# Kernel optimization log

Measured on AMD Instinct MI355X. Metric: run time of the kernel, lower is better.

Reference implementation:

```python
import jax, jax.numpy as jnp
import numpy as np

N, E, IN, HID, OUT = 100000, 1600000, 128, 128, 64


def _gcn(x, w, b, src, dst, norm, n):
    # PyG GCNConv: linear transform, then normalized scatter-add aggregation
    h = x @ w                                  # [N, F_out]
    msg = h[src] * norm[:, None]               # gather + scale, [E', F_out]
    agg = jax.ops.segment_sum(msg, dst, num_segments=n)
    return agg + b


def setup_inputs() -> dict:
    key = jax.random.key(0)
    ks = jax.random.split(key, 10)
    s = 0.05
    return {
        "X": jax.random.normal(ks[0], (N, IN), jnp.float32),
        "edge_index": jax.random.randint(ks[1], (2, E), 0, N, jnp.int64),
        "unused": 0,
        "gw1": jax.random.normal(ks[2], (IN, HID), jnp.float32) * s,
        "gb1": jnp.zeros((HID,), jnp.float32),
        "lw1": jax.random.normal(ks[3], (IN, HID), jnp.float32) * s,
        "lb1": jnp.zeros((HID,), jnp.float32),
        "gw2": jax.random.normal(ks[4], (HID, HID), jnp.float32) * s,
        "gb2": jnp.zeros((HID,), jnp.float32),
        "lw2": jax.random.normal(ks[5], (HID, HID), jnp.float32) * s,
        "lb2": jnp.zeros((HID,), jnp.float32),
        "gw3": jax.random.normal(ks[6], (HID, HID), jnp.float32) * s,
        "gb3": jnp.zeros((HID,), jnp.float32),
        "lw3": jax.random.normal(ks[7], (HID, HID), jnp.float32) * s,
        "lb3": jnp.zeros((HID,), jnp.float32),
        "fcw": jax.random.normal(ks[8], (HID, OUT), jnp.float32) * s,
        "fcb": jnp.zeros((OUT,), jnp.float32),
    }


def reference(X, edge_index, unused, gw1, gb1, lw1, lb1, gw2, gb2, lw2, lb2,
              gw3, gb3, lw3, lb3, fcw, fcb):
    n = X.shape[0]
    loop = jnp.arange(n)
    src = jnp.concatenate([edge_index[0], loop])   # self-loops appended
    dst = jnp.concatenate([edge_index[1], loop])
    deg = jax.ops.segment_sum(jnp.ones_like(dst, dtype=X.dtype), dst, num_segments=n)
    dis = jnp.where(deg > 0, jax.lax.rsqrt(jnp.maximum(deg, 1e-12)), 0.0)
    norm = dis[src] * dis[dst]                     # D^-1/2 (A+I) D^-1/2 weights

    lrelu = lambda v: jax.nn.leaky_relu(v, negative_slope=0.01)
    h = lrelu(_gcn(X, gw1, gb1, src, dst, norm, n) + X @ lw1 + lb1)
    h = lrelu(_gcn(h, gw2, gb2, src, dst, norm, n) + h @ lw2 + lb2)
    h = lrelu(_gcn(h, gw3, gb3, src, dst, norm, n) + h @ lw3 + lb3)
    y = h @ fcw + fcb
    return (h, y)
```

## Files before the change

### kernel.cpp

```cpp
#include <hip/hip_runtime.h>
#include <cstdint>
#include <cstddef>


typedef __attribute__((ext_vector_type(4))) float f32x4;
typedef __attribute__((ext_vector_type(8))) short bf16x8;
typedef unsigned short u16;

#define G_CHUNKS 256

__device__ __forceinline__ float bf2f(unsigned int u) {
  union { unsigned int i; float f; } v;
  v.i = u << 16;
  return v.f;
}
__device__ __forceinline__ u16 f2bf(float f) {
  union { float f; unsigned int i; } v;
  v.f = f;
  unsigned int i = v.i;
  return (u16)((i + 0x7FFFu + ((i >> 16) & 1u)) >> 16);
}


__global__ __launch_bounds__(256) void k_hist(const int* __restrict__ ei,
                                              int* __restrict__ ghist,
                                              int E, int B, int chunk) {
  __shared__ int h[512];
  for (int t = threadIdx.x; t < B; t += 256) h[t] = 0;
  __syncthreads();
  const int g = blockIdx.x;
  const int beg = g * chunk;
  const int end = min(beg + chunk, E);
  for (int e = beg + threadIdx.x; e < end; e += 256)
    atomicAdd(&h[ei[E + e] >> 8], 1);
  __syncthreads();
  for (int t = threadIdx.x; t < B; t += 256) ghist[(size_t)t * G_CHUNKS + g] = h[t];
}

__global__ __launch_bounds__(256) void k_hscan(int* __restrict__ ghist,
                                               int* __restrict__ btot) {
  __shared__ int sm[256];
  int* p = ghist + (size_t)blockIdx.x * G_CHUNKS;
  const int t = threadIdx.x;
  int v = p[t];
  sm[t] = v;
  __syncthreads();
  for (int off = 1; off < 256; off <<= 1) {
    int u = (t >= off) ? sm[t - off] : 0;
    __syncthreads();
    sm[t] += u;
    __syncthreads();
  }
  p[t] = sm[t] - v;
  if (t == 255) btot[blockIdx.x] = sm[255];
}

__global__ __launch_bounds__(512) void k_bscan(const int* __restrict__ btot,
                                               int* __restrict__ boff, int B,
                                               int* __restrict__ rowptr, int n,
                                               int E, int tot) {
  __shared__ int sm[512];
  const int t = threadIdx.x;
  int v = (t < B) ? btot[t] : 0;
  sm[t] = v;
  __syncthreads();
  for (int off = 1; off < 512; off <<= 1) {
    int u = (t >= off) ? sm[t - off] : 0;
    __syncthreads();
    sm[t] += u;
    __syncthreads();
  }
  if (t < B) boff[t] = sm[t] - v;
  if (t == 0) {
    boff[B] = E;
    rowptr[n] = tot;
  }
}

__global__ __launch_bounds__(256) void k_scatter(const int* __restrict__ ei,
                                                 const int* __restrict__ ghist,
                                                 const int* __restrict__ boff,
                                                 unsigned int* __restrict__ ebuf,
                                                 int E, int B, int chunk) {
  __shared__ int off[512];
  const int g = blockIdx.x;
  for (int t = threadIdx.x; t < B; t += 256)
    off[t] = boff[t] + ghist[(size_t)t * G_CHUNKS + g];
  __syncthreads();
  const int beg = g * chunk;
  const int end = min(beg + chunk, E);
  for (int e = beg + threadIdx.x; e < end; e += 256) {
    int s = ei[e];
    int d = ei[E + e];
    int pos = atomicAdd(&off[d >> 8], 1);
    ebuf[pos] = ((unsigned int)s << 8) | (unsigned int)(d & 255);
  }
}

__global__ __launch_bounds__(256) void k_cfill(const unsigned int* __restrict__ ebuf,
                                               const int* __restrict__ boff,
                                               int* __restrict__ rowptr,
                                               int* __restrict__ col,
                                               float* __restrict__ dis, int n) {
  __shared__ int cnt[256];
  __shared__ int fl[256];
  const int b = blockIdx.x;
  const int t = threadIdx.x;
  const int beg = boff[b];
  const int end = boff[b + 1];
  const int node0 = b << 8;
  const int nn = min(256, n - node0);
  cnt[t] = 0;
  __syncthreads();
  for (int e = beg + t; e < end; e += 256)
    atomicAdd(&cnt[ebuf[e] & 255u], 1);
  __syncthreads();
  int v = cnt[t];
  __shared__ int sm[256];
  sm[t] = v;
  __syncthreads();
  for (int off = 1; off < 256; off <<= 1) {
    int u = (t >= off) ? sm[t - off] : 0;
    __syncthreads();
    sm[t] += u;
    __syncthreads();
  }
  if (t < nn) {
    int excl = sm[t] - v;
    int rbase = beg + node0 + t + excl;
    int i = node0 + t;
    rowptr[i] = rbase;
    col[rbase] = i;
    fl[t] = rbase + 1;
    dis[i] = rsqrtf((float)(v + 1));
  }
  __syncthreads();
  for (int e = beg + t; e < end; e += 256) {
    unsigned int pk = ebuf[e];
    int pos = atomicAdd(&fl[pk & 255u], 1);
    col[pos] = (int)(pk >> 8);
  }
}


__global__ __launch_bounds__(256) void k_cvt(const float* __restrict__ src,
                                             u16* __restrict__ dst, int total8) {
  int i = blockIdx.x * 256 + threadIdx.x;
  if (i >= total8) return;
  size_t b = (size_t)i * 8;
  float4 a0 = *(const float4*)(src + b);
  float4 a1 = *(const float4*)(src + b + 4);
  u16 o[8] = {f2bf(a0.x), f2bf(a0.y), f2bf(a0.z), f2bf(a0.w),
              f2bf(a1.x), f2bf(a1.y), f2bf(a1.z), f2bf(a1.w)};
  *(ulonglong2*)(dst + b) = *(ulonglong2*)o;
}

__global__ __launch_bounds__(128) void k_prep(const float* __restrict__ w0,
                                              const float* __restrict__ w1,
                                              const float* __restrict__ w2,
                                              const float* __restrict__ w3,
                                              const float* __restrict__ w4,
                                              const float* __restrict__ w5,
                                              const float* __restrict__ g1,
                                              const float* __restrict__ l1,
                                              const float* __restrict__ g2,
                                              const float* __restrict__ l2,
                                              const float* __restrict__ g3,
                                              const float* __restrict__ l3,
                                              const float* __restrict__ fcw,
                                              u16* __restrict__ wt,
                                              float* __restrict__ bias,
                                              u16* __restrict__ fcT) {
  int bx = blockIdx.x;
  if (bx < 768) {
    int z = bx >> 7, nr = bx & 127, k = threadIdx.x;
    const float* Ws[6] = {w0, w1, w2, w3, w4, w5};
    wt[(size_t)z * 16384 + nr * 128 + k] = f2bf(Ws[z][k * 128 + nr]);
  } else if (bx < 771) {
    int t = (bx - 768) * 128 + threadIdx.x;
    if (t < 384) {
      const float* gs[3] = {g1, g2, g3};
      const float* ls[3] = {l1, l2, l3};
      bias[t] = gs[t >> 7][t & 127] + ls[t >> 7][t & 127];
    }
  } else {
    int nr = bx - 771;
    int k = threadIdx.x;
    fcT[nr * 128 + k] = f2bf(fcw[k * 64 + nr]);
  }
}

__global__ __launch_bounds__(256) void k_spmv_bf(const int* __restrict__ rowptr,
                                                 const int* __restrict__ col,
                                                 const float* __restrict__ dis,
                                                 const u16* __restrict__ Xb,
                                                 u16* __restrict__ SXb, int n) {
  const int wave = threadIdx.x >> 6;
  const int lane = threadIdx.x & 63;
  const int i = blockIdx.x * 4 + wave;
  if (i >= n) return;
  int j = rowptr[i];
  const int end = rowptr[i + 1];
  float ax = 0.f, ay = 0.f;

  for (; (j & 3) && j < end; ++j) {
    int c0 = col[j];
    float w0 = dis[c0];
    unsigned int q0 = *(const unsigned int*)(Xb + (size_t)c0 * 128 + lane * 2);
    ax = fmaf(bf2f(q0 & 0xffffu), w0, ax);
    ay = fmaf(bf2f(q0 >> 16), w0, ay);
  }
  for (; j + 3 < end; j += 4) {
    int4 c4 = *(const int4*)(col + j);
    float w0 = dis[c4.x], w1 = dis[c4.y], w2 = dis[c4.z], w3 = dis[c4.w];
    unsigned int q0 = *(const unsigned int*)(Xb + (size_t)c4.x * 128 + lane * 2);
    unsigned int q1 = *(const unsigned int*)(Xb + (size_t)c4.y * 128 + lane * 2);
    unsigned int q2 = *(const unsigned int*)(Xb + (size_t)c4.z * 128 + lane * 2);
    unsigned int q3 = *(const unsigned int*)(Xb + (size_t)c4.w * 128 + lane * 2);
    ax = fmaf(bf2f(q0 & 0xffffu), w0, ax);
    ay = fmaf(bf2f(q0 >> 16), w0, ay);
    ax = fmaf(bf2f(q1 & 0xffffu), w1, ax);
    ay = fmaf(bf2f(q1 >> 16), w1, ay);
    ax = fmaf(bf2f(q2 & 0xffffu), w2, ax);
    ay = fmaf(bf2f(q2 >> 16), w2, ay);
    ax = fmaf(bf2f(q3 & 0xffffu), w3, ax);
    ay = fmaf(bf2f(q3 >> 16), w3, ay);
  }
  for (; j < end; ++j) {
    int c0 = col[j];
    float w0 = dis[c0];
    unsigned int q0 = *(const unsigned int*)(Xb + (size_t)c0 * 128 + lane * 2);
    ax = fmaf(bf2f(q0 & 0xffffu), w0, ax);
    ay = fmaf(bf2f(q0 >> 16), w0, ay);
  }
  float di = dis[i];
  ax *= di;
  ay *= di;
  unsigned int o = (unsigned int)f2bf(ax) | ((unsigned int)f2bf(ay) << 16);
  *(unsigned int*)(SXb + (size_t)i * 128 + lane * 2) = o;
}

__global__ __launch_bounds__(256) void k_mfma(const u16* __restrict__ A0,
                                              const u16* __restrict__ A1,
                                              const u16* __restrict__ W0T,
                                              const u16* __restrict__ W1T,
                                              const float* __restrict__ bias,
                                              u16* __restrict__ outb,
                                              float* __restrict__ outf, int M) {
  const int lane = threadIdx.x & 63;
  const int wv = threadIdx.x >> 6;
  const int row0 = blockIdx.x * 128 + wv * 32;
  const int r = lane & 15;
  const int kg = lane >> 4;

  f32x4 acc[2][8];
#pragma unroll
  for (int a = 0; a < 2; ++a)
#pragma unroll
    for (int j = 0; j < 8; ++j) acc[a][j] = (f32x4){0.f, 0.f, 0.f, 0.f};

  const int ra0 = min(row0 + r, M - 1);
  const int ra1 = min(row0 + 16 + r, M - 1);

#pragma unroll
  for (int p = 0; p < 2; ++p) {
    const u16* A = p ? A1 : A0;
    const u16* WT = p ? W1T : W0T;
#pragma unroll
    for (int kk = 0; kk < 4; ++kk) {
      const int k0 = kk * 32 + kg * 8;
      bf16x8 a0 = *(const bf16x8*)(A + (size_t)ra0 * 128 + k0);
      bf16x8 a1 = *(const bf16x8*)(A + (size_t)ra1 * 128 + k0);
#pragma unroll
      for (int j = 0; j < 8; ++j) {
        bf16x8 b = *(const bf16x8*)(WT + (size_t)(j * 16 + r) * 128 + k0);
        acc[0][j] = __builtin_amdgcn_mfma_f32_16x16x32_bf16(a0, b, acc[0][j], 0, 0, 0);
        acc[1][j] = __builtin_amdgcn_mfma_f32_16x16x32_bf16(a1, b, acc[1][j], 0, 0, 0);
      }
    }
  }

#pragma unroll
  for (int rf = 0; rf < 2; ++rf)
#pragma unroll
    for (int e = 0; e < 4; ++e) {
      const int row = row0 + rf * 16 + kg * 4 + e;
      if (row >= M) continue;
#pragma unroll
      for (int j = 0; j < 8; ++j) {
        const int c = j * 16 + r;
        float v = acc[rf][j][e] + bias[c];
        v = (v > 0.f) ? v : 0.01f * v;
        if (outf) outf[(size_t)row * 128 + c] = v;
        if (outb) outb[(size_t)row * 128 + c] = f2bf(v);
      }
    }
}

__global__ __launch_bounds__(256) void k_fc_mfma(const u16* __restrict__ hb3,
                                                 const u16* __restrict__ fcT,
                                                 const float* __restrict__ fcb,
                                                 float* __restrict__ y, int M) {
  const int lane = threadIdx.x & 63;
  const int wv = threadIdx.x >> 6;
  const int row0 = blockIdx.x * 128 + wv * 32;
  const int r = lane & 15;
  const int kg = lane >> 4;

  f32x4 acc[2][4];
#pragma unroll
  for (int a = 0; a < 2; ++a)
#pragma unroll
    for (int j = 0; j < 4; ++j) acc[a][j] = (f32x4){0.f, 0.f, 0.f, 0.f};

  const int ra0 = min(row0 + r, M - 1);
  const int ra1 = min(row0 + 16 + r, M - 1);

#pragma unroll
  for (int kk = 0; kk < 4; ++kk) {
    const int k0 = kk * 32 + kg * 8;
    bf16x8 a0 = *(const bf16x8*)(hb3 + (size_t)ra0 * 128 + k0);
    bf16x8 a1 = *(const bf16x8*)(hb3 + (size_t)ra1 * 128 + k0);
#pragma unroll
    for (int j = 0; j < 4; ++j) {
      bf16x8 b = *(const bf16x8*)(fcT + (size_t)(j * 16 + r) * 128 + k0);
      acc[0][j] = __builtin_amdgcn_mfma_f32_16x16x32_bf16(a0, b, acc[0][j], 0, 0, 0);
      acc[1][j] = __builtin_amdgcn_mfma_f32_16x16x32_bf16(a1, b, acc[1][j], 0, 0, 0);
    }
  }

#pragma unroll
  for (int rf = 0; rf < 2; ++rf)
#pragma unroll
    for (int e = 0; e < 4; ++e) {
      const int row = row0 + rf * 16 + kg * 4 + e;
      if (row >= M) continue;
#pragma unroll
      for (int j = 0; j < 4; ++j) {
        const int c = j * 16 + r;
        y[(size_t)row * 64 + c] = acc[rf][j][e] + fcb[c];
      }
    }
}


extern "C" void kernel_launch(void* const* d_in, const int* in_sizes, int n_in,
                              void* d_out, int out_size, void* d_ws, size_t ws_size,
                              hipStream_t stream) {
  const float* X  = (const float*)d_in[0];
  const int* ei   = (const int*)d_in[1];
  const float* gw1 = (const float*)d_in[3];
  const float* gb1 = (const float*)d_in[4];
  const float* lw1 = (const float*)d_in[5];
  const float* lb1 = (const float*)d_in[6];
  const float* gw2 = (const float*)d_in[7];
  const float* gb2 = (const float*)d_in[8];
  const float* lw2 = (const float*)d_in[9];
  const float* lb2 = (const float*)d_in[10];
  const float* gw3 = (const float*)d_in[11];
  const float* gb3 = (const float*)d_in[12];
  const float* lw3 = (const float*)d_in[13];
  const float* lb3 = (const float*)d_in[14];
  const float* fcw = (const float*)d_in[15];
  const float* fcb = (const float*)d_in[16];

  const int n = in_sizes[0] / 128;
  const int E = in_sizes[1] / 2;
  const int tot = E + n;
  const int B = (n + 255) >> 8;
  const int chunk = (E + G_CHUNKS - 1) / G_CHUNKS;

  char* ws = (char*)d_ws;
  size_t off = 0;
  auto alloc = [&](size_t bytes) -> void* {
    void* p = ws + off;
    off = (off + bytes + 255) & ~(size_t)255;
    return p;
  };
  int* ghist   = (int*)alloc((size_t)B * G_CHUNKS * 4);
  int* btot    = (int*)alloc(512 * 4);
  int* boff    = (int*)alloc((size_t)(B + 1) * 4);
  int* rowptr  = (int*)alloc((size_t)(n + 1) * 4);
  float* dis   = (float*)alloc((size_t)n * 4);
  int* col     = (int*)alloc((size_t)tot * 4);
  unsigned int* ebuf = (unsigned int*)alloc((size_t)E * 4);
  u16* Xb      = (u16*)alloc((size_t)n * 128 * 2);
  u16* SXb     = (u16*)alloc((size_t)n * 128 * 2);
  u16* WT      = (u16*)alloc((size_t)6 * 16384 * 2);
  u16* fcT     = (u16*)alloc((size_t)64 * 128 * 2);
  float* bias  = (float*)alloc(384 * 4);

  float* outh = (float*)d_out;
  float* outy = outh + (size_t)n * 128;
  u16* hb = (u16*)outy;

  const int gM = (n + 127) / 128;
  const int gW = (n + 3) / 4;
  const int g8 = (n * 128 / 8 + 255) / 256;

  k_hist<<<G_CHUNKS, 256, 0, stream>>>(ei, ghist, E, B, chunk);
  k_hscan<<<B, 256, 0, stream>>>(ghist, btot);
  k_bscan<<<1, 512, 0, stream>>>(btot, boff, B, rowptr, n, E, tot);
  k_scatter<<<G_CHUNKS, 256, 0, stream>>>(ei, ghist, boff, ebuf, E, B, chunk);
  k_cfill<<<B, 256, 0, stream>>>(ebuf, boff, rowptr, col, dis, n);

  k_cvt<<<g8, 256, 0, stream>>>(X, Xb, n * 128 / 8);
  k_prep<<<835, 128, 0, stream>>>(gw1, lw1, gw2, lw2, gw3, lw3,
                                  gb1, lb1, gb2, lb2, gb3, lb3, fcw,
                                  WT, bias, fcT);

  k_spmv_bf<<<gW, 256, 0, stream>>>(rowptr, col, dis, Xb, SXb, n);
  k_mfma<<<gM, 256, 0, stream>>>(SXb, Xb, WT, WT + 16384, bias, hb, nullptr, n);
  k_spmv_bf<<<gW, 256, 0, stream>>>(rowptr, col, dis, hb, SXb, n);
  k_mfma<<<gM, 256, 0, stream>>>(SXb, hb, WT + 2 * 16384, WT + 3 * 16384,
                                 bias + 128, hb, nullptr, n);
  k_spmv_bf<<<gW, 256, 0, stream>>>(rowptr, col, dis, hb, SXb, n);
  k_mfma<<<gM, 256, 0, stream>>>(SXb, hb, WT + 4 * 16384, WT + 5 * 16384,
                                 bias + 256, Xb, outh, n);
  k_fc_mfma<<<gM, 256, 0, stream>>>(Xb, fcT, fcb, outy, n);
}
```

Baseline: 522.5 us.

## Fuse SpMV aggregation into MFMA layer kernel via swizzled LDS tile

Merges the per-layer SpMV gather kernel and the dense MFMA kernel into one k_layer kernel. Each block aggregates its 128 rows into a swizzled 32KB shared-memory tile, then feeds that tile straight into the MFMA stage. This removes the global write and re-read of the intermediate SX buffer and one launch per layer. The cost is that only 782 blocks of 256 threads do the irregular gather, down from 25k small blocks, so latency hiding for the gather may suffer. A separate h2b buffer is added so a layer never reads and writes the same array.

```diff
diff --git a/kernel.cpp b/kernel.cpp
--- a/kernel.cpp
+++ b/kernel.cpp
@@ -190,66 +190,68 @@
   }
 }
 
-__global__ __launch_bounds__(256) void k_spmv_bf(const int* __restrict__ rowptr,
-                                                 const int* __restrict__ col,
-                                                 const float* __restrict__ dis,
-                                                 const u16* __restrict__ Xb,
-                                                 u16* __restrict__ SXb, int n) {
-  const int wave = threadIdx.x >> 6;
-  const int lane = threadIdx.x & 63;
-  const int i = blockIdx.x * 4 + wave;
-  if (i >= n) return;
-  int j = rowptr[i];
-  const int end = rowptr[i + 1];
-  float ax = 0.f, ay = 0.f;
-
-  for (; (j & 3) && j < end; ++j) {
-    int c0 = col[j];
-    float w0 = dis[c0];
-    unsigned int q0 = *(const unsigned int*)(Xb + (size_t)c0 * 128 + lane * 2);
-    ax = fmaf(bf2f(q0 & 0xffffu), w0, ax);
-    ay = fmaf(bf2f(q0 >> 16), w0, ay);
-  }
-  for (; j + 3 < end; j += 4) {
-    int4 c4 = *(const int4*)(col + j);
-    float w0 = dis[c4.x], w1 = dis[c4.y], w2 = dis[c4.z], w3 = dis[c4.w];
-    unsigned int q0 = *(const unsigned int*)(Xb + (size_t)c4.x * 128 + lane * 2);
-    unsigned int q1 = *(const unsigned int*)(Xb + (size_t)c4.y * 128 + lane * 2);
-    unsigned int q2 = *(const unsigned int*)(Xb + (size_t)c4.z * 128 + lane * 2);
-    unsigned int q3 = *(const unsigned int*)(Xb + (size_t)c4.w * 128 + lane * 2);
-    ax = fmaf(bf2f(q0 & 0xffffu), w0, ax);
-    ay = fmaf(bf2f(q0 >> 16), w0, ay);
-    ax = fmaf(bf2f(q1 & 0xffffu), w1, ax);
-    ay = fmaf(bf2f(q1 >> 16), w1, ay);
-    ax = fmaf(bf2f(q2 & 0xffffu), w2, ax);
-    ay = fmaf(bf2f(q2 >> 16), w2, ay);
-    ax = fmaf(bf2f(q3 & 0xffffu), w3, ax);
-    ay = fmaf(bf2f(q3 >> 16), w3, ay);
-  }
-  for (; j < end; ++j) {
-    int c0 = col[j];
-    float w0 = dis[c0];
-    unsigned int q0 = *(const unsigned int*)(Xb + (size_t)c0 * 128 + lane * 2);
-    ax = fmaf(bf2f(q0 & 0xffffu), w0, ax);
-    ay = fmaf(bf2f(q0 >> 16), w0, ay);
-  }
-  float di = dis[i];
-  ax *= di;
-  ay *= di;
-  unsigned int o = (unsigned int)f2bf(ax) | ((unsigned int)f2bf(ay) << 16);
-  *(unsigned int*)(SXb + (size_t)i * 128 + lane * 2) = o;
-}
-
-__global__ __launch_bounds__(256) void k_mfma(const u16* __restrict__ A0,
-                                              const u16* __restrict__ A1,
-                                              const u16* __restrict__ W0T,
-                                              const u16* __restrict__ W1T,
-                                              const float* __restrict__ bias,
-                                              u16* __restrict__ outb,
-                                              float* __restrict__ outf, int M) {
+__global__ __launch_bounds__(256, 4) void k_layer(const int* __restrict__ rowptr,
+                                                  const int* __restrict__ col,
+                                                  const float* __restrict__ dis,
+                                                  const u16* __restrict__ Ab,
+                                                  const u16* __restrict__ W0T,
+                                                  const u16* __restrict__ W1T,
+                                                  const float* __restrict__ bias,
+                                                  u16* __restrict__ outb,
+                                                  float* __restrict__ outf,
+                                                  int n) {
+  __shared__ char ldsb[128 * 256];
   const int lane = threadIdx.x & 63;
   const int wv = threadIdx.x >> 6;
-  const int row0 = blockIdx.x * 128 + wv * 32;
+  const int row0 = blockIdx.x * 128;
+
+  for (int t = 0; t < 32; ++t) {
+    const int li = wv * 32 + t;
+    const int i = row0 + li;
+    float ax = 0.f, ay = 0.f;
+    if (i < n) {
+      int j = rowptr[i];
+      const int end = rowptr[i + 1];
+      for (; (j & 3) && j < end; ++j) {
+        int c0 = col[j];
+        float w0 = dis[c0];
+        unsigned int q0 = *(const unsigned int*)(Ab + (size_t)c0 * 128 + lane * 2);
+        ax = fmaf(bf2f(q0 & 0xffffu), w0, ax);
+        ay = fmaf(bf2f(q0 >> 16), w0, ay);
+      }
+      for (; j + 3 < end; j += 4) {
+        int4 c4 = *(const int4*)(col + j);
+        float w0 = dis[c4.x], w1 = dis[c4.y], w2 = dis[c4.z], w3 = dis[c4.w];
+        unsigned int q0 = *(const unsigned int*)(Ab + (size_t)c4.x * 128 + lane * 2);
+        unsigned int q1 = *(const unsigned int*)(Ab + (size_t)c4.y * 128 + lane * 2);
+        unsigned int q2 = *(const unsigned int*)(Ab + (size_t)c4.z * 128 + lane * 2);
+        unsigned int q3 = *(const unsigned int*)(Ab + (size_t)c4.w * 128 + lane * 2);
+        ax = fmaf(bf2f(q0 & 0xffffu), w0, ax);
+        ay = fmaf(bf2f(q0 >> 16), w0, ay);
+        ax = fmaf(bf2f(q1 & 0xffffu), w1, ax);
+        ay = fmaf(bf2f(q1 >> 16), w1, ay);
+        ax = fmaf(bf2f(q2 & 0xffffu), w2, ax);
+        ay = fmaf(bf2f(q2 >> 16), w2, ay);
+        ax = fmaf(bf2f(q3 & 0xffffu), w3, ax);
+        ay = fmaf(bf2f(q3 >> 16), w3, ay);
+      }
+      for (; j < end; ++j) {
+        int c0 = col[j];
+        float w0 = dis[c0];
+        unsigned int q0 = *(const unsigned int*)(Ab + (size_t)c0 * 128 + lane * 2);
+        ax = fmaf(bf2f(q0 & 0xffffu), w0, ax);
+        ay = fmaf(bf2f(q0 >> 16), w0, ay);
+      }
+      float di = dis[i];
+      ax *= di;
+      ay *= di;
+    }
+    unsigned int o = (unsigned int)f2bf(ax) | ((unsigned int)f2bf(ay) << 16);
+    const int kbyte = lane * 4;
+    *(unsigned int*)(ldsb + li * 256 + (kbyte ^ ((li & 7) << 4))) = o;
+  }
+  __syncthreads();
+
   const int r = lane & 15;
   const int kg = lane >> 4;
 
@@ -259,24 +261,35 @@
 #pragma unroll
     for (int j = 0; j < 8; ++j) acc[a][j] = (f32x4){0.f, 0.f, 0.f, 0.f};
 
-  const int ra0 = min(row0 + r, M - 1);
-  const int ra1 = min(row0 + 16 + r, M - 1);
-
-#pragma unroll
-  for (int p = 0; p < 2; ++p) {
-    const u16* A = p ? A1 : A0;
-    const u16* WT = p ? W1T : W0T;
-#pragma unroll
-    for (int kk = 0; kk < 4; ++kk) {
-      const int k0 = kk * 32 + kg * 8;
-      bf16x8 a0 = *(const bf16x8*)(A + (size_t)ra0 * 128 + k0);
-      bf16x8 a1 = *(const bf16x8*)(A + (size_t)ra1 * 128 + k0);
-#pragma unroll
-      for (int j = 0; j < 8; ++j) {
-        bf16x8 b = *(const bf16x8*)(WT + (size_t)(j * 16 + r) * 128 + k0);
-        acc[0][j] = __builtin_amdgcn_mfma_f32_16x16x32_bf16(a0, b, acc[0][j], 0, 0, 0);
-        acc[1][j] = __builtin_amdgcn_mfma_f32_16x16x32_bf16(a1, b, acc[1][j], 0, 0, 0);
-      }
+  const int lr0 = wv * 32 + r;
+  const int lr1 = wv * 32 + 16 + r;
+  const int ra0 = min(row0 + lr0, n - 1);
+  const int ra1 = min(row0 + lr1, n - 1);
+  const int sw = (r & 7) << 4;
+
+#pragma unroll
+  for (int kk = 0; kk < 4; ++kk) {
+    const int kb = kk * 64 + kg * 16;
+    bf16x8 a0 = *(const bf16x8*)(ldsb + lr0 * 256 + (kb ^ sw));
+    bf16x8 a1 = *(const bf16x8*)(ldsb + lr1 * 256 + (kb ^ sw));
+    const int k0 = kk * 32 + kg * 8;
+#pragma unroll
+    for (int j = 0; j < 8; ++j) {
+      bf16x8 b = *(const bf16x8*)(W0T + (size_t)(j * 16 + r) * 128 + k0);
+      acc[0][j] = __builtin_amdgcn_mfma_f32_16x16x32_bf16(a0, b, acc[0][j], 0, 0, 0);
+      acc[1][j] = __builtin_amdgcn_mfma_f32_16x16x32_bf16(a1, b, acc[1][j], 0, 0, 0);
+    }
+  }
+#pragma unroll
+  for (int kk = 0; kk < 4; ++kk) {
+    const int k0 = kk * 32 + kg * 8;
+    bf16x8 a0 = *(const bf16x8*)(Ab + (size_t)ra0 * 128 + k0);
+    bf16x8 a1 = *(const bf16x8*)(Ab + (size_t)ra1 * 128 + k0);
+#pragma unroll
+    for (int j = 0; j < 8; ++j) {
+      bf16x8 b = *(const bf16x8*)(W1T + (size_t)(j * 16 + r) * 128 + k0);
+      acc[0][j] = __builtin_amdgcn_mfma_f32_16x16x32_bf16(a0, b, acc[0][j], 0, 0, 0);
+      acc[1][j] = __builtin_amdgcn_mfma_f32_16x16x32_bf16(a1, b, acc[1][j], 0, 0, 0);
     }
   }
 
@@ -284,8 +297,8 @@
   for (int rf = 0; rf < 2; ++rf)
 #pragma unroll
     for (int e = 0; e < 4; ++e) {
-      const int row = row0 + rf * 16 + kg * 4 + e;
-      if (row >= M) continue;
+      const int row = row0 + wv * 32 + rf * 16 + kg * 4 + e;
+      if (row >= n) continue;
 #pragma unroll
       for (int j = 0; j < 8; ++j) {
         const int c = j * 16 + r;
@@ -385,7 +398,7 @@
   int* col     = (int*)alloc((size_t)tot * 4);
   unsigned int* ebuf = (unsigned int*)alloc((size_t)E * 4);
   u16* Xb      = (u16*)alloc((size_t)n * 128 * 2);
-  u16* SXb     = (u16*)alloc((size_t)n * 128 * 2);
+  u16* h2b     = (u16*)alloc((size_t)n * 128 * 2);
   u16* WT      = (u16*)alloc((size_t)6 * 16384 * 2);
   u16* fcT     = (u16*)alloc((size_t)64 * 128 * 2);
   float* bias  = (float*)alloc(384 * 4);
@@ -395,7 +408,6 @@
   u16* hb = (u16*)outy;
 
   const int gM = (n + 127) / 128;
-  const int gW = (n + 3) / 4;
   const int g8 = (n * 128 / 8 + 255) / 256;
 
   k_hist<<<G_CHUNKS, 256, 0, stream>>>(ei, ghist, E, B, chunk);
@@ -409,13 +421,13 @@
                                   gb1, lb1, gb2, lb2, gb3, lb3, fcw,
                                   WT, bias, fcT);
 
-  k_spmv_bf<<<gW, 256, 0, stream>>>(rowptr, col, dis, Xb, SXb, n);
-  k_mfma<<<gM, 256, 0, stream>>>(SXb, Xb, WT, WT + 16384, bias, hb, nullptr, n);
-  k_spmv_bf<<<gW, 256, 0, stream>>>(rowptr, col, dis, hb, SXb, n);
-  k_mfma<<<gM, 256, 0, stream>>>(SXb, hb, WT + 2 * 16384, WT + 3 * 16384,
-                                 bias + 128, hb, nullptr, n);
-  k_spmv_bf<<<gW, 256, 0, stream>>>(rowptr, col, dis, hb, SXb, n);
-  k_mfma<<<gM, 256, 0, stream>>>(SXb, hb, WT + 4 * 16384, WT + 5 * 16384,
-                                 bias + 256, Xb, outh, n);
+  k_layer<<<gM, 256, 0, stream>>>(rowptr, col, dis, Xb,
+                                  WT, WT + 16384, bias, hb, nullptr, n);
+  k_layer<<<gM, 256, 0, stream>>>(rowptr, col, dis, hb,
+                                  WT + 2 * 16384, WT + 3 * 16384, bias + 128,
+                                  h2b, nullptr, n);
+  k_layer<<<gM, 256, 0, stream>>>(rowptr, col, dis, h2b,
+                                  WT + 4 * 16384, WT + 5 * 16384, bias + 256,
+                                  Xb, outh, n);
   k_fc_mfma<<<gM, 256, 0, stream>>>(Xb, fcT, fcb, outy, n);
 }
```

After: 669.5 us. 1.28x slower.

## Pre-scale features by source degree norm to drop per-edge dis gathers in SpMV

Applied to the files above, without the earlier changes.

The converter and the MFMA epilogue now also write a copy of the features pre-multiplied by each row's D^-1/2 factor. The SpMV can then just sum neighbour rows without gathering dis[col] per edge. The SpMV inner loop is also unrolled to 8 edges with launch bounds that hint occupancy. This trades an extra bf16 write of the full feature matrix per layer, plus rounding after scaling, for removing a dependent scattered load per edge.

```diff
diff --git a/kernel.cpp b/kernel.cpp
--- a/kernel.cpp
+++ b/kernel.cpp
@@ -144,15 +144,21 @@
 
 
 __global__ __launch_bounds__(256) void k_cvt(const float* __restrict__ src,
-                                             u16* __restrict__ dst, int total8) {
+                                             const float* __restrict__ dis,
+                                             u16* __restrict__ dstb,
+                                             u16* __restrict__ dsts, int total8) {
   int i = blockIdx.x * 256 + threadIdx.x;
   if (i >= total8) return;
   size_t b = (size_t)i * 8;
+  float ds = dis[i >> 4];
   float4 a0 = *(const float4*)(src + b);
   float4 a1 = *(const float4*)(src + b + 4);
-  u16 o[8] = {f2bf(a0.x), f2bf(a0.y), f2bf(a0.z), f2bf(a0.w),
-              f2bf(a1.x), f2bf(a1.y), f2bf(a1.z), f2bf(a1.w)};
-  *(ulonglong2*)(dst + b) = *(ulonglong2*)o;
+  u16 ob[8] = {f2bf(a0.x), f2bf(a0.y), f2bf(a0.z), f2bf(a0.w),
+               f2bf(a1.x), f2bf(a1.y), f2bf(a1.z), f2bf(a1.w)};
+  u16 os[8] = {f2bf(a0.x * ds), f2bf(a0.y * ds), f2bf(a0.z * ds), f2bf(a0.w * ds),
+               f2bf(a1.x * ds), f2bf(a1.y * ds), f2bf(a1.z * ds), f2bf(a1.w * ds)};
+  *(ulonglong2*)(dstb + b) = *(ulonglong2*)ob;
+  *(ulonglong2*)(dsts + b) = *(ulonglong2*)os;
 }
 
 __global__ __launch_bounds__(128) void k_prep(const float* __restrict__ w0,
@@ -190,11 +196,11 @@
   }
 }
 
-__global__ __launch_bounds__(256) void k_spmv_bf(const int* __restrict__ rowptr,
-                                                 const int* __restrict__ col,
-                                                 const float* __restrict__ dis,
-                                                 const u16* __restrict__ Xb,
-                                                 u16* __restrict__ SXb, int n) {
+__global__ __launch_bounds__(256, 4) void k_spmv_bf(const int* __restrict__ rowptr,
+                                                    const int* __restrict__ col,
+                                                    const float* __restrict__ dis,
+                                                    const u16* __restrict__ Xs,
+                                                    u16* __restrict__ SXb, int n) {
   const int wave = threadIdx.x >> 6;
   const int lane = threadIdx.x & 63;
   const int i = blockIdx.x * 4 + wave;
@@ -203,36 +209,29 @@
   const int end = rowptr[i + 1];
   float ax = 0.f, ay = 0.f;
 
-  for (; (j & 3) && j < end; ++j) {
-    int c0 = col[j];
-    float w0 = dis[c0];
-    unsigned int q0 = *(const unsigned int*)(Xb + (size_t)c0 * 128 + lane * 2);
-    ax = fmaf(bf2f(q0 & 0xffffu), w0, ax);
-    ay = fmaf(bf2f(q0 >> 16), w0, ay);
-  }
-  for (; j + 3 < end; j += 4) {
-    int4 c4 = *(const int4*)(col + j);
-    float w0 = dis[c4.x], w1 = dis[c4.y], w2 = dis[c4.z], w3 = dis[c4.w];
-    unsigned int q0 = *(const unsigned int*)(Xb + (size_t)c4.x * 128 + lane * 2);
-    unsigned int q1 = *(const unsigned int*)(Xb + (size_t)c4.y * 128 + lane * 2);
-    unsigned int q2 = *(const unsigned int*)(Xb + (size_t)c4.z * 128 + lane * 2);
-    unsigned int q3 = *(const unsigned int*)(Xb + (size_t)c4.w * 128 + lane * 2);
-    ax = fmaf(bf2f(q0 & 0xffffu), w0, ax);
-    ay = fmaf(bf2f(q0 >> 16), w0, ay);
-    ax = fmaf(bf2f(q1 & 0xffffu), w1, ax);
-    ay = fmaf(bf2f(q1 >> 16), w1, ay);
-    ax = fmaf(bf2f(q2 & 0xffffu), w2, ax);
-    ay = fmaf(bf2f(q2 >> 16), w2, ay);
-    ax = fmaf(bf2f(q3 & 0xffffu), w3, ax);
-    ay = fmaf(bf2f(q3 >> 16), w3, ay);
-  }
-  for (; j < end; ++j) {
-    int c0 = col[j];
-    float w0 = dis[c0];
-    unsigned int q0 = *(const unsigned int*)(Xb + (size_t)c0 * 128 + lane * 2);
-    ax = fmaf(bf2f(q0 & 0xffffu), w0, ax);
-    ay = fmaf(bf2f(q0 >> 16), w0, ay);
-  }
+#define ROWQ(c) (*(const unsigned int*)(Xs + (size_t)(c) * 128 + lane * 2))
+#define ACC(q)  do { unsigned int _q = (q); \
+                     ax += bf2f(_q & 0xffffu); ay += bf2f(_q >> 16); } while (0)
+
+  for (; (j & 3) && j < end; ++j) ACC(ROWQ(col[j]));
+  for (; j + 7 < end; j += 8) {
+    int4 c0 = *(const int4*)(col + j);
+    int4 c1 = *(const int4*)(col + j + 4);
+    unsigned int q0 = ROWQ(c0.x), q1 = ROWQ(c0.y), q2 = ROWQ(c0.z), q3 = ROWQ(c0.w);
+    unsigned int q4 = ROWQ(c1.x), q5 = ROWQ(c1.y), q6 = ROWQ(c1.z), q7 = ROWQ(c1.w);
+    ACC(q0); ACC(q1); ACC(q2); ACC(q3);
+    ACC(q4); ACC(q5); ACC(q6); ACC(q7);
+  }
+  if (j + 3 < end) {
+    int4 c0 = *(const int4*)(col + j);
+    unsigned int q0 = ROWQ(c0.x), q1 = ROWQ(c0.y), q2 = ROWQ(c0.z), q3 = ROWQ(c0.w);
+    ACC(q0); ACC(q1); ACC(q2); ACC(q3);
+    j += 4;
+  }
+  for (; j < end; ++j) ACC(ROWQ(col[j]));
+#undef ROWQ
+#undef ACC
+
   float di = dis[i];
   ax *= di;
   ay *= di;
@@ -245,7 +244,9 @@
                                               const u16* __restrict__ W0T,
                                               const u16* __restrict__ W1T,
                                               const float* __restrict__ bias,
+                                              const float* __restrict__ dis,
                                               u16* __restrict__ outb,
+                                              u16* __restrict__ outs,
                                               float* __restrict__ outf, int M) {
   const int lane = threadIdx.x & 63;
   const int wv = threadIdx.x >> 6;
@@ -286,6 +287,7 @@
     for (int e = 0; e < 4; ++e) {
       const int row = row0 + rf * 16 + kg * 4 + e;
       if (row >= M) continue;
+      const float ds = outs ? dis[row] : 0.f;
 #pragma unroll
       for (int j = 0; j < 8; ++j) {
         const int c = j * 16 + r;
@@ -293,6 +295,7 @@
         v = (v > 0.f) ? v : 0.01f * v;
         if (outf) outf[(size_t)row * 128 + c] = v;
         if (outb) outb[(size_t)row * 128 + c] = f2bf(v);
+        if (outs) outs[(size_t)row * 128 + c] = f2bf(v * ds);
       }
     }
 }
@@ -385,6 +388,7 @@
   int* col     = (int*)alloc((size_t)tot * 4);
   unsigned int* ebuf = (unsigned int*)alloc((size_t)E * 4);
   u16* Xb      = (u16*)alloc((size_t)n * 128 * 2);
+  u16* Xs      = (u16*)alloc((size_t)n * 128 * 2);
   u16* SXb     = (u16*)alloc((size_t)n * 128 * 2);
   u16* WT      = (u16*)alloc((size_t)6 * 16384 * 2);
   u16* fcT     = (u16*)alloc((size_t)64 * 128 * 2);
@@ -404,18 +408,19 @@
   k_scatter<<<G_CHUNKS, 256, 0, stream>>>(ei, ghist, boff, ebuf, E, B, chunk);
   k_cfill<<<B, 256, 0, stream>>>(ebuf, boff, rowptr, col, dis, n);
 
-  k_cvt<<<g8, 256, 0, stream>>>(X, Xb, n * 128 / 8);
+  k_cvt<<<g8, 256, 0, stream>>>(X, dis, Xb, Xs, n * 128 / 8);
   k_prep<<<835, 128, 0, stream>>>(gw1, lw1, gw2, lw2, gw3, lw3,
                                   gb1, lb1, gb2, lb2, gb3, lb3, fcw,
                                   WT, bias, fcT);
 
-  k_spmv_bf<<<gW, 256, 0, stream>>>(rowptr, col, dis, Xb, SXb, n);
-  k_mfma<<<gM, 256, 0, stream>>>(SXb, Xb, WT, WT + 16384, bias, hb, nullptr, n);
-  k_spmv_bf<<<gW, 256, 0, stream>>>(rowptr, col, dis, hb, SXb, n);
+  k_spmv_bf<<<gW, 256, 0, stream>>>(rowptr, col, dis, Xs, SXb, n);
+  k_mfma<<<gM, 256, 0, stream>>>(SXb, Xb, WT, WT + 16384, bias, dis,
+                                 hb, Xs, nullptr, n);
+  k_spmv_bf<<<gW, 256, 0, stream>>>(rowptr, col, dis, Xs, SXb, n);
   k_mfma<<<gM, 256, 0, stream>>>(SXb, hb, WT + 2 * 16384, WT + 3 * 16384,
-                                 bias + 128, hb, nullptr, n);
-  k_spmv_bf<<<gW, 256, 0, stream>>>(rowptr, col, dis, hb, SXb, n);
+                                 bias + 128, dis, hb, Xs, nullptr, n);
+  k_spmv_bf<<<gW, 256, 0, stream>>>(rowptr, col, dis, Xs, SXb, n);
   k_mfma<<<gM, 256, 0, stream>>>(SXb, hb, WT + 4 * 16384, WT + 5 * 16384,
-                                 bias + 256, Xb, outh, n);
+                                 bias + 256, dis, Xb, nullptr, outh, n);
   k_fc_mfma<<<gM, 256, 0, stream>>>(Xb, fcT, fcb, outy, n);
 }
```

New measurement: 508.0 us. -2.8%, faster.
